# Kernel optimization log

Measured on AMD Instinct MI355X. Metric: run time of the kernel, lower is better.

## Reference

```python
import jax, jax.numpy as jnp
import numpy as np

# Dims: B nodes, Z species (elements), IN/OUT channels, M = 2*l+1 (l=1)
B, Z, IN, OUT, M = 8192, 10, 512, 512, 3
ALPHA = 1.0 / np.sqrt(IN)  # self.alpha = 1/sqrt(in_dim)
SQRT3 = float(np.sqrt(3.0))


def setup_inputs() -> dict:
    key = jax.random.key(0)
    k1, k2, k3 = jax.random.split(key, 3)
    t = jax.random.normal(k1, (B, IN, M), dtype=jnp.float32)
    species = jax.random.randint(k2, (B,), 0, Z)
    node_attrs = jax.nn.one_hot(species, Z, dtype=jnp.float32)  # [B, Z] one-hot
    # torch.nn.init.uniform_(weights, -sqrt(3), sqrt(3))
    weights = jax.random.uniform(k3, (Z, OUT, IN), dtype=jnp.float32,
                                 minval=-SQRT3, maxval=SQRT3)
    return {"t": t, "node_attrs": node_attrs, "weights": weights}


def reference(t, node_attrs, weights):
    # Faithful to: einsum('bz, zCc, bcd -> bCd', node_attrs, weights*alpha, t)
    # Contract weights with t first per species ([Z,B,C,M], ~500MB), which
    # avoids the huge [B,C,c] per-node weight-gather intermediate, then
    # select/sum over species with the one-hot node_attrs.
    W = weights * ALPHA                       # [Z, OUT, IN]
    zt = jnp.einsum('zCc,bcd->zbCd', W, t)    # [Z, B, OUT, M]
    out = jnp.einsum('bz,zbCd->bCd', node_attrs, zt)  # [B, OUT, M]
    return out
```

## Files before the change

kernel.cpp:

```cpp
#include <hip/hip_runtime.h>
#include <stdint.h>

#define NB   8192
#define NZ   10
#define CIN  512
#define COUT 512
#define MM   3
#define ALPHA 0.04419417382415922f

#define ROWS_TOTAL (NB * MM)
#define BM 128
#define BN 128
#define BK 32
#define KITERS (CIN / BK)
#define MAX_MT (ROWS_TOTAL / BM + NZ)
#define NGRP 32

typedef short bf16x8 __attribute__((ext_vector_type(8)));
typedef float f32x4  __attribute__((ext_vector_type(4)));

__device__ __forceinline__ uint16_t f2bf(float f) {
    union { float f; uint32_t i; } v; v.f = f;
    uint32_t x = v.i;
    x += 0x7fffu + ((x >> 16) & 1u);
    return (uint16_t)(x >> 16);
}
__device__ __forceinline__ uint32_t pack2(float a, float b) {
    return (uint32_t)f2bf(a) | ((uint32_t)f2bf(b) << 16);
}
__device__ __forceinline__ void async16(const ushort* g, ushort* l) {
    __builtin_amdgcn_global_load_lds((const uint32_t*)g, (uint32_t*)l, 16, 0, 0);
}

__global__ __launch_bounds__(256)
void prep_kernel(const float* __restrict__ attrs, const float* __restrict__ w,
                 int* __restrict__ species, int* __restrict__ hist,
                 ushort* __restrict__ wt) {
    const int tid = threadIdx.x;
    if (blockIdx.x >= NGRP) {
        const size_t i = ((size_t)(blockIdx.x - NGRP) * 256 + tid) * 8;
        float4 a = *(const float4*)(w + i);
        float4 b = *(const float4*)(w + i + 4);
        uint4 o;
        o.x = pack2(a.x, a.y); o.y = pack2(a.z, a.w);
        o.z = pack2(b.x, b.y); o.w = pack2(b.z, b.w);
        *(uint4*)(wt + i) = o;
        return;
    }
    __shared__ int wc[4][NZ];
    const int b = blockIdx.x * 256 + tid;
    const float* a = attrs + (size_t)b * NZ;
    int s = 0;
    #pragma unroll
    for (int z = 0; z < NZ; z++) if (a[z] > 0.5f) s = z;
    species[b] = s;
    const int wv = tid >> 6, lane = tid & 63;
    #pragma unroll
    for (int z = 0; z < NZ; z++) {
        unsigned long long m = __ballot(s == z);
        if (lane == 0) wc[wv][z] = __popcll(m);
    }
    __syncthreads();
    if (tid < NZ) {
        hist[blockIdx.x * NZ + tid] = wc[0][tid] + wc[1][tid] + wc[2][tid] + wc[3][tid];
    }
}

__global__ __launch_bounds__(256)
void place_kernel(const int* __restrict__ species, const int* __restrict__ hist,
                  int* __restrict__ sorted, int* __restrict__ offsets,
                  int* __restrict__ tile_offsets) {
    __shared__ int lhist[NGRP][NZ];
    __shared__ int loff[NZ + 1], ltoff[NZ + 1];
    __shared__ int pb[NZ];
    __shared__ int wc[4][NZ];
    const int tid = threadIdx.x, g = blockIdx.x;

    for (int i = tid; i < NGRP * NZ; i += 256) ((int*)lhist)[i] = hist[i];
    __syncthreads();
    if (tid == 0) {
        int off = 0, toff = 0;
        for (int z = 0; z < NZ; z++) {
            int tot = 0;
            for (int gg = 0; gg < NGRP; gg++) tot += lhist[gg][z];
            loff[z] = off; ltoff[z] = toff;
            off += tot;
            toff += (3 * tot + BM - 1) / BM;
        }
        loff[NZ] = off; ltoff[NZ] = toff;
    }
    __syncthreads();
    if (tid < NZ) {
        int base = loff[tid];
        for (int gg = 0; gg < g; gg++) base += lhist[gg][tid];
        pb[tid] = base;
    }
    if (g == 0 && tid < NZ + 1) {
        offsets[tid] = loff[tid];
        tile_offsets[tid] = ltoff[tid];
    }
    const int b = g * 256 + tid;
    const int s = species[b];
    const int wv = tid >> 6, lane = tid & 63;
    unsigned long long mymask = 0;
    #pragma unroll
    for (int z = 0; z < NZ; z++) {
        unsigned long long m = __ballot(s == z);
        if (lane == 0) wc[wv][z] = __popcll(m);
        if (s == z) mymask = m;
    }
    __syncthreads();
    int rank = __popcll(mymask & ((1ull << lane) - 1ull));
    #pragma unroll
    for (int w2 = 0; w2 < 4; w2++) if (w2 < wv) rank += wc[w2][s];
    sorted[pb[s] + rank] = b;
}

__global__ __launch_bounds__(256)
void pack_t(const float* __restrict__ t, const int* __restrict__ sorted,
            ushort* __restrict__ tt) {
    const int w = threadIdx.x >> 6, L = threadIdx.x & 63;
    const int p = blockIdx.x * 4 + w;
    const int node = sorted[p];
    const float4* src = (const float4*)(t + (size_t)node * (CIN * MM) + L * 24);
    float4 f[6];
    #pragma unroll
    for (int i = 0; i < 6; i++) f[i] = src[i];
    const float* v = (const float*)f;
    #pragma unroll
    for (int d = 0; d < MM; d++) {
        uint4 o;
        o.x = pack2(v[d],      v[3 + d]);
        o.y = pack2(v[6 + d],  v[9 + d]);
        o.z = pack2(v[12 + d], v[15 + d]);
        o.w = pack2(v[18 + d], v[21 + d]);
        *(uint4*)&tt[(size_t)(3 * p + d) * CIN + L * 8] = o;
    }
}

__global__ __launch_bounds__(256)
void gemm_kernel(const ushort* __restrict__ tt, const ushort* __restrict__ wt,
                 const int* __restrict__ sorted, const int* __restrict__ offsets,
                 const int* __restrict__ tile_offsets, float* __restrict__ out) {
    __shared__ ushort As[2][BK / 8][BM][8];
    __shared__ ushort Bs[2][BK / 8][BN][8];
    __shared__ int spos[48];

    const int tz = blockIdx.x;
    if (tz >= tile_offsets[NZ]) return;
    int z = 0;
    #pragma unroll
    for (int i = 1; i < NZ; i++) if (tile_offsets[i] <= tz) z = i;

    const int row_base = 3 * offsets[z] + (tz - tile_offsets[z]) * BM;
    const int row_end  = 3 * offsets[z + 1];
    const int pos0     = row_base / 3;
    const int Cbase    = blockIdx.y * BN;

    const int tid = threadIdx.x;
    const int w = tid >> 6, L = tid & 63;

    if (tid < 48) spos[tid] = sorted[min(pos0 + tid, NB - 1)];

    const ushort* gA0 = tt + (size_t)(row_base + L) * CIN + w * 8;
    const ushort* gA1 = gA0 + (size_t)64 * CIN;
    const ushort* gB0 = wt + ((size_t)z * COUT + Cbase + L) * CIN + w * 8;
    const ushort* gB1 = gB0 + (size_t)64 * CIN;

    const int wm = w & 1, wn = w >> 1;
    const int q = L >> 4, mr = L & 15;

    f32x4 acc[4][4];
    #pragma unroll
    for (int i = 0; i < 4; i++)
        #pragma unroll
        for (int j = 0; j < 4; j++) acc[i][j] = (f32x4){0.f, 0.f, 0.f, 0.f};

#define STAGE(bufi, ko) do {                       \
        async16(gA0 + (ko), &As[bufi][w][0][0]);   \
        async16(gA1 + (ko), &As[bufi][w][64][0]);  \
        async16(gB0 + (ko), &Bs[bufi][w][0][0]);   \
        async16(gB1 + (ko), &Bs[bufi][w][64][0]);  \
    } while (0)

    STAGE(0, 0);
    __syncthreads();

    for (int kt = 0; kt < KITERS; kt++) {
        const int cur = kt & 1;
        if (kt + 1 < KITERS) STAGE(cur ^ 1, (kt + 1) * BK);

        bf16x8 af[4], bf[4];
        #pragma unroll
        for (int am = 0; am < 4; am++)
            af[am] = *(const bf16x8*)&As[cur][q][wm * 64 + am * 16 + mr][0];
        #pragma unroll
        for (int bn = 0; bn < 4; bn++)
            bf[bn] = *(const bf16x8*)&Bs[cur][q][wn * 64 + bn * 16 + mr][0];
        #pragma unroll
        for (int am = 0; am < 4; am++)
            #pragma unroll
            for (int bn = 0; bn < 4; bn++)
                acc[am][bn] = __builtin_amdgcn_mfma_f32_16x16x32_bf16(
                    af[am], bf[bn], acc[am][bn], 0, 0, 0);

        __syncthreads();
    }
#undef STAGE

    #pragma unroll
    for (int am = 0; am < 4; am++) {
        #pragma unroll
        for (int r = 0; r < 4; r++) {
            const int Rg = row_base + wm * 64 + am * 16 + q * 4 + r;
            if (Rg < row_end) {
                const int pos = Rg / 3;
                const int d = Rg - 3 * pos;
                const int node = spos[pos - pos0];
                float* o = out + (size_t)node * (COUT * MM) + d;
                #pragma unroll
                for (int bn = 0; bn < 4; bn++) {
                    const int Cg = Cbase + wn * 64 + bn * 16 + mr;
                    o[(size_t)Cg * 3] = ALPHA * acc[am][bn][r];
                }
            }
        }
    }
}

extern "C" void kernel_launch(void* const* d_in, const int* in_sizes, int n_in,
                              void* d_out, int out_size, void* d_ws, size_t ws_size,
                              hipStream_t stream) {
    const float* t     = (const float*)d_in[0];
    const float* attrs = (const float*)d_in[1];
    const float* w     = (const float*)d_in[2];
    float* out = (float*)d_out;

    uint8_t* ws = (uint8_t*)d_ws;
    int* species      = (int*)ws;                  ws += NB * 4;
    int* sorted       = (int*)ws;                  ws += NB * 4;
    int* hist         = (int*)ws;                  ws += NGRP * NZ * 4;
    int* offsets      = (int*)ws;                  ws += 16 * 4;
    int* tile_offsets = (int*)ws;                  ws += 16 * 4;
    ws = (uint8_t*)(((uintptr_t)ws + 255) & ~(uintptr_t)255);
    ushort* wt = (ushort*)ws;                      ws += (size_t)NZ * COUT * CIN * 2;
    ushort* tt = (ushort*)ws;

    hipLaunchKernelGGL(prep_kernel, dim3(NGRP + (NZ * COUT * CIN) / 2048), dim3(256),
                       0, stream, attrs, w, species, hist, wt);
    hipLaunchKernelGGL(place_kernel, dim3(NGRP), dim3(256), 0, stream,
                       species, hist, sorted, offsets, tile_offsets);
    hipLaunchKernelGGL(pack_t, dim3(NB / 4), dim3(256), 0, stream, t, sorted, tt);
    hipLaunchKernelGGL(gemm_kernel, dim3(MAX_MT, COUT / BN), dim3(256), 0, stream,
                       tt, wt, sorted, offsets, tile_offsets, out);
}
```

Measured before the change: 159.7 us.

## Swizzle GEMM LDS layout, remap workgroups, stage epilogue through LDS, fine-grained waits

Rewrites the GEMM LDS layout as row-major tiles with an XOR swizzle on the k-chunk, which is meant to avoid bank conflicts on fragment reads and make global loads more contiguous per row. Moves to a 1D grid with a workgroup-to-tile remap so neighbouring blocks spread across XCDs and share tiles in cache. Replaces __syncthreads with explicit vmcnt waits plus raw barriers so the next stage's loads stay in flight. Rewrites the epilogue to stage outputs through LDS in three chunks so each node's row is written with coalesced stores instead of stride-3 scattered writes. The weight-cast prep kernel also changes its per-thread access pattern. The cost is extra barriers and an LDS round trip in the epilogue.

```diff
diff --git a/kernel.cpp b/kernel.cpp
--- a/kernel.cpp
+++ b/kernel.cpp
@@ -14,6 +14,8 @@
 #define BK 32
 #define KITERS (CIN / BK)
 #define MAX_MT (ROWS_TOTAL / BM + NZ)
+#define NYB (COUT / BN)
+#define NWG (MAX_MT * NYB)
 #define NGRP 32
 
 typedef short bf16x8 __attribute__((ext_vector_type(8)));
@@ -28,7 +30,7 @@
 __device__ __forceinline__ uint32_t pack2(float a, float b) {
     return (uint32_t)f2bf(a) | ((uint32_t)f2bf(b) << 16);
 }
-__device__ __forceinline__ void async16(const ushort* g, ushort* l) {
+__device__ __forceinline__ void async16(const void* g, void* l) {
     __builtin_amdgcn_global_load_lds((const uint32_t*)g, (uint32_t*)l, 16, 0, 0);
 }
 
@@ -38,13 +40,16 @@
                  ushort* __restrict__ wt) {
     const int tid = threadIdx.x;
     if (blockIdx.x >= NGRP) {
-        const size_t i = ((size_t)(blockIdx.x - NGRP) * 256 + tid) * 8;
-        float4 a = *(const float4*)(w + i);
-        float4 b = *(const float4*)(w + i + 4);
-        uint4 o;
-        o.x = pack2(a.x, a.y); o.y = pack2(a.z, a.w);
-        o.z = pack2(b.x, b.y); o.w = pack2(b.z, b.w);
-        *(uint4*)(wt + i) = o;
+        const size_t base = (size_t)(blockIdx.x - NGRP) * 2048;
+        const float* src = w + base;
+        ushort* dst = wt + base;
+        float4 a = *(const float4*)(src + tid * 4);
+        float4 b = *(const float4*)(src + 1024 + tid * 4);
+        uint2 oa, ob;
+        oa.x = pack2(a.x, a.y); oa.y = pack2(a.z, a.w);
+        ob.x = pack2(b.x, b.y); ob.y = pack2(b.z, b.w);
+        *(uint2*)(dst + tid * 4) = oa;
+        *(uint2*)(dst + 1024 + tid * 4) = ob;
         return;
     }
     __shared__ int wc[4][NZ];
@@ -142,11 +147,14 @@
 void gemm_kernel(const ushort* __restrict__ tt, const ushort* __restrict__ wt,
                  const int* __restrict__ sorted, const int* __restrict__ offsets,
                  const int* __restrict__ tile_offsets, float* __restrict__ out) {
-    __shared__ ushort As[2][BK / 8][BM][8];
-    __shared__ ushort Bs[2][BK / 8][BN][8];
+    __shared__ __align__(16) ushort smem[2][2][BM][BK];
     __shared__ int spos[48];
 
-    const int tz = blockIdx.x;
+    const int bid = blockIdx.x;
+    const int nid = (bid & 7) * (NWG / 8) + (bid >> 3);
+    const int tz = nid >> 2;
+    const int Cbase = (nid & 3) * BN;
+
     if (tz >= tile_offsets[NZ]) return;
     int z = 0;
     #pragma unroll
@@ -155,20 +163,20 @@
     const int row_base = 3 * offsets[z] + (tz - tile_offsets[z]) * BM;
     const int row_end  = 3 * offsets[z + 1];
     const int pos0     = row_base / 3;
-    const int Cbase    = blockIdx.y * BN;
 
     const int tid = threadIdx.x;
     const int w = tid >> 6, L = tid & 63;
-
     if (tid < 48) spos[tid] = sorted[min(pos0 + tid, NB - 1)];
 
-    const ushort* gA0 = tt + (size_t)(row_base + L) * CIN + w * 8;
-    const ushort* gA1 = gA0 + (size_t)64 * CIN;
-    const ushort* gB0 = wt + ((size_t)z * COUT + Cbase + L) * CIN + w * 8;
-    const ushort* gB1 = gB0 + (size_t)64 * CIN;
+    const int lr = L >> 2;
+    const int cs = (L & 3) ^ ((L >> 3) & 3);
+    const int soff = lr * CIN + cs * 8;
+    const ushort* gA = tt + (size_t)(row_base + w * 32) * CIN + soff;
+    const ushort* gB = wt + ((size_t)z * COUT + Cbase + w * 32) * CIN + soff;
 
     const int wm = w & 1, wn = w >> 1;
     const int q = L >> 4, mr = L & 15;
+    const int sr8 = (q ^ ((mr >> 1) & 3)) * 8;
 
     f32x4 acc[4][4];
     #pragma unroll
@@ -176,27 +184,31 @@
         #pragma unroll
         for (int j = 0; j < 4; j++) acc[i][j] = (f32x4){0.f, 0.f, 0.f, 0.f};
 
-#define STAGE(bufi, ko) do {                       \
-        async16(gA0 + (ko), &As[bufi][w][0][0]);   \
-        async16(gA1 + (ko), &As[bufi][w][64][0]);  \
-        async16(gB0 + (ko), &Bs[bufi][w][0][0]);   \
-        async16(gB1 + (ko), &Bs[bufi][w][64][0]);  \
+#define STAGE(bufi, ko) do {                                        \
+        async16(gA + (ko),                  &smem[0][bufi][w * 32][0]);      \
+        async16(gA + 16 * CIN + (ko),       &smem[0][bufi][w * 32 + 16][0]); \
+        async16(gB + (ko),                  &smem[1][bufi][w * 32][0]);      \
+        async16(gB + 16 * CIN + (ko),       &smem[1][bufi][w * 32 + 16][0]); \
     } while (0)
 
     STAGE(0, 0);
-    __syncthreads();
-
     for (int kt = 0; kt < KITERS; kt++) {
         const int cur = kt & 1;
-        if (kt + 1 < KITERS) STAGE(cur ^ 1, (kt + 1) * BK);
+        if (kt + 1 < KITERS) {
+            STAGE(cur ^ 1, (kt + 1) * BK);
+            asm volatile("s_waitcnt vmcnt(4)" ::: "memory");
+        } else {
+            asm volatile("s_waitcnt vmcnt(0)" ::: "memory");
+        }
+        asm volatile("s_barrier" ::: "memory");
 
         bf16x8 af[4], bf[4];
         #pragma unroll
         for (int am = 0; am < 4; am++)
-            af[am] = *(const bf16x8*)&As[cur][q][wm * 64 + am * 16 + mr][0];
+            af[am] = *(const bf16x8*)&smem[0][cur][wm * 64 + am * 16 + mr][sr8];
         #pragma unroll
         for (int bn = 0; bn < 4; bn++)
-            bf[bn] = *(const bf16x8*)&Bs[cur][q][wn * 64 + bn * 16 + mr][0];
+            bf[bn] = *(const bf16x8*)&smem[1][cur][wn * 64 + bn * 16 + mr][sr8];
         #pragma unroll
         for (int am = 0; am < 4; am++)
             #pragma unroll
@@ -204,25 +216,44 @@
                 acc[am][bn] = __builtin_amdgcn_mfma_f32_16x16x32_bf16(
                     af[am], bf[bn], acc[am][bn], 0, 0, 0);
 
+        asm volatile("s_barrier" ::: "memory");
+    }
+#undef STAGE
+
+    float* ebuf = (float*)smem;
+    #pragma unroll
+    for (int ch = 0; ch < 3; ch++) {
         __syncthreads();
-    }
-#undef STAGE
-
-    #pragma unroll
-    for (int am = 0; am < 4; am++) {
-        #pragma unroll
-        for (int r = 0; r < 4; r++) {
-            const int Rg = row_base + wm * 64 + am * 16 + q * 4 + r;
-            if (Rg < row_end) {
+        const int pbase = pos0 + ch * 16;
+        #pragma unroll
+        for (int am = 0; am < 4; am++) {
+            #pragma unroll
+            for (int r = 0; r < 4; r++) {
+                const int Rg = row_base + wm * 64 + am * 16 + q * 4 + r;
                 const int pos = Rg / 3;
                 const int d = Rg - 3 * pos;
+                const int lp = pos - pbase;
+                if (lp >= 0 && lp < 16 && Rg < row_end) {
+                    #pragma unroll
+                    for (int bn = 0; bn < 4; bn++) {
+                        const int c = wn * 64 + bn * 16 + mr;
+                        ebuf[(lp * BN + c) * 3 + d] = ALPHA * acc[am][bn][r];
+                    }
+                }
+            }
+        }
+        __syncthreads();
+        #pragma unroll 4
+        for (int j = 0; j < 24; j++) {
+            const int idx = j * 256 + tid;
+            const int lp  = idx / 384;
+            const int o   = idx - lp * 384;
+            const int pos = pbase + lp;
+            const int d   = o % 3;
+            const int row = 3 * pos + d;
+            if (row >= row_base && row < row_base + BM && row < row_end) {
                 const int node = spos[pos - pos0];
-                float* o = out + (size_t)node * (COUT * MM) + d;
-                #pragma unroll
-                for (int bn = 0; bn < 4; bn++) {
-                    const int Cg = Cbase + wn * 64 + bn * 16 + mr;
-                    o[(size_t)Cg * 3] = ALPHA * acc[am][bn][r];
-                }
+                out[(size_t)node * (COUT * MM) + Cbase * 3 + o] = ebuf[idx];
             }
         }
     }
@@ -251,6 +282,6 @@
     hipLaunchKernelGGL(place_kernel, dim3(NGRP), dim3(256), 0, stream,
                        species, hist, sorted, offsets, tile_offsets);
     hipLaunchKernelGGL(pack_t, dim3(NB / 4), dim3(256), 0, stream, t, sorted, tt);
-    hipLaunchKernelGGL(gemm_kernel, dim3(MAX_MT, COUT / BN), dim3(256), 0, stream,
+    hipLaunchKernelGGL(gemm_kernel, dim3(NWG), dim3(256), 0, stream,
                        tt, wt, sorted, offsets, tile_offsets, out);
 }
```

New measurement: 152.7 us. -4.4%, faster.
